# Optimization experiments

Measured on AMD Instinct MI355X. Metric: run time of the kernel, lower is better.

Reference implementation:

```python
import jax, jax.numpy as jnp
import numpy as np

B, L, D, V = 4096, 200, 64, 100000
ATTR_LEN = (2, 6, 10)  # label_size = 18
NEG = -1e9


def setup_inputs() -> dict:
    key = jax.random.key(0)
    ks = jax.random.split(key, 12)
    x = jax.random.randint(ks[0], (B, L), 0, V)
    lengths = jax.random.randint(ks[1], (B,), 1, L + 1)  # ragged valid lengths >= 1
    x_mask = jnp.arange(L)[None, :] < lengths[:, None]   # prefix-valid bool mask [B,L]
    y = (jax.random.uniform(ks[2], (B, sum(ATTR_LEN))) < 0.5).astype(jnp.float32)
    ob = (jax.random.uniform(ks[3], (B, sum(ATTR_LEN))) < 0.8).astype(jnp.float32)
    emb_table = (jax.random.normal(ks[4], (V, D)) * 0.02).at[0].set(0.0)  # padding_idx=0
    tran_W = jax.random.normal(ks[5], (3, D, D)) * 0.05   # emb_tran Linear weights (per attr)
    tran_b = jnp.zeros((3, D))
    att_W = jax.random.normal(ks[6], (3, D)) * 0.05       # item_att_W: Linear(D,1) per attr
    att_b = jnp.zeros((3,))
    W0 = jax.random.normal(ks[7], (D, ATTR_LEN[0])) * 0.05  # W_all (no bias)
    W1 = jax.random.normal(ks[8], (D, ATTR_LEN[1])) * 0.05
    W2 = jax.random.normal(ks[9], (D, ATTR_LEN[2])) * 0.05
    return {"x": x, "x_mask": x_mask, "y": y, "ob": ob, "emb_table": emb_table,
            "tran_W": tran_W, "tran_b": tran_b, "att_W": att_W, "att_b": att_b,
            "W0": W0, "W1": W1, "W2": W2}


def reference(x, x_mask, y, ob, emb_table, tran_W, tran_b, att_W, att_b, W0, W1, W2):
    # embed: [B,L,D]
    embed = emb_table[x]
    # per-attribute transformed embeddings: [3,B,L,D]
    e = jax.nn.relu(jnp.einsum('bld,ade->able', embed, tran_W) + tran_b[:, None, None, :])
    # attention logits per attribute: [3,B,L]
    att_u = jax.nn.relu(jnp.einsum('able,ae->abl', e, att_W) + att_b[:, None, None])
    # masked softmax over valid prefix (equivalent to the per-sample length loop)
    m = x_mask.astype(e.dtype)
    scores = jnp.where(x_mask[None, :, :], att_u, NEG)
    att = jax.nn.softmax(scores, axis=-1) * m[None, :, :]
    # attention-pooled user representation per attribute: [3,B,D]
    rep = jnp.tanh(jnp.einsum('abl,able->abe', att, e))
    # torch: cat([rep_a.unsqueeze(2)],2).view(B,-1) -> interleaved (d-major, attr-minor) layout
    user_flat = jnp.transpose(rep, (1, 2, 0)).reshape(rep.shape[1], -1)  # [B, 3*D]
    Ddim = emb_table.shape[1]
    W_user = jnp.concatenate([user_flat[:, 0 * Ddim:1 * Ddim] @ W0,
                              user_flat[:, 1 * Ddim:2 * Ddim] @ W1,
                              user_flat[:, 2 * Ddim:3 * Ddim] @ W2], axis=1)
    # W_compact = W_user * ob  (observed-label mask)
    return W_user * ob
```

## Files before the change

### kernel.cpp

```cpp
#include <hip/hip_runtime.h>

typedef unsigned int u32;
typedef unsigned short u16;
typedef unsigned char u8;
typedef unsigned long long u64;

typedef __attribute__((ext_vector_type(8))) short bf16x8;
typedef __attribute__((ext_vector_type(4))) float f32x4;
typedef __attribute__((ext_vector_type(4))) u32 u32x4;

#define L_SEQ 200
#define ST_ROWS 208
#define RND_MAX 9

__device__ __forceinline__ u16 f2bf(float f) {
    u32 u = __float_as_uint(f);
    return (u16)((u + 0x7FFFu + ((u >> 16) & 1u)) >> 16);
}
__device__ __forceinline__ u32 pk2bf(float fx, float fy) {
    u32 xb = __float_as_uint(fx) + 0x8000u;
    u32 yb = __float_as_uint(fy) + 0x8000u;
    return __byte_perm(xb, yb, 0x7632);
}

__device__ __forceinline__ float row16_sum(float v) {
    int x;
    x = __builtin_amdgcn_update_dpp(0, __float_as_int(v), 0x128, 0xF, 0xF, true);
    v += __int_as_float(x);
    x = __builtin_amdgcn_update_dpp(0, __float_as_int(v), 0x124, 0xF, 0xF, true);
    v += __int_as_float(x);
    x = __builtin_amdgcn_update_dpp(0, __float_as_int(v), 0x122, 0xF, 0xF, true);
    v += __int_as_float(x);
    x = __builtin_amdgcn_update_dpp(0, __float_as_int(v), 0x121, 0xF, 0xF, true);
    v += __int_as_float(x);
    return v;
}
__device__ __forceinline__ float wave_sumf(float v) {
    v = row16_sum(v);
    v += __shfl_xor(v, 16, 64);
    v += __shfl_xor(v, 32, 64);
    return v;
}

__global__ __launch_bounds__(256) void etna_prep(const void* __restrict__ xmask,
                                                 const float* __restrict__ tranW,
                                                 const float* __restrict__ emb,
                                                 void* __restrict__ ws, int Bn, int Vn,
                                                 int doConv) {
    const int tid = threadIdx.x;
    const int bid = blockIdx.x;

    if (doConv) {
        u64* dst = (u64*)((char*)ws + 40960);
        const float4* src = (const float4*)emb;
        int ng = Vn * 16;
        for (int i = bid * 256 + tid; i < ng; i += gridDim.x * 256) {
            float4 v = src[i];
            u64 lo = pk2bf(v.x, v.y);
            u64 hi = pk2bf(v.z, v.w);
            dst[i] = lo | (hi << 32);
        }
    }

    if (bid < 48) {
        int it = bid * 256 + tid;
        int jj = it & 7;
        int ln = (it >> 3) & 63;
        int kh = (it >> 9) & 1;
        int c = (it >> 10) & 3;
        int a = it >> 12;
        int k = kh * 32 + (ln >> 4) * 8 + jj;
        int n = c * 16 + (ln & 15);
        ((u16*)ws)[it] = f2bf(tranW[a * 4096 + k * 64 + n]);
        return;
    }

    const int wv = tid >> 6;
    const int lane = tid & 63;
    int esz;
    {
        u32 accF = 0, acc0 = 0, accO = 0;
#pragma unroll
        for (int k = 0; k < 4; ++k) {
            int i = lane + 64 * k;
            u32 w = (i < 200) ? ((const u32*)xmask)[i] : 0u;
            accF |= (w & 0xFEFEFEFEu);
            acc0 |= (w & 0x000000FFu);
            accO |= (w & 0xFFFFFF00u);
        }
        bool isFloat = __ballot(accF != 0) != 0;
        bool hasB0   = __ballot(acc0 != 0) != 0;
        bool hasOdd  = __ballot(accO != 0) != 0;
        esz = isFloat ? (hasB0 ? 2 : 4) : (hasOdd ? 1 : 4);
    }
    int s = (bid - 48) * 4 + wv;
    if (s < Bn) {
        int len = 0;
        int mbase = s * L_SEQ;
#pragma unroll
        for (int c4 = 0; c4 < 4; ++c4) {
            int l = c4 * 64 + lane;
            bool v = false;
            if (l < L_SEQ) {
                int off = mbase + l;
                if (esz == 1)      v = ((const u8*)xmask)[off] != 0;
                else if (esz == 2) v = ((const u16*)xmask)[off] != 0;
                else               v = ((const u32*)xmask)[off] != 0;
            }
            len += (int)__popcll(__ballot(v));
        }
        if (lane == 0) ((int*)((char*)ws + 24576))[s] = len;
    }
}

template <bool TAB>
__global__ __launch_bounds__(192, 4) void etna_mfma(
    const int* __restrict__ x, const float* __restrict__ ob,
    const float* __restrict__ emb, const float* __restrict__ tranb,
    const float* __restrict__ attW, const float* __restrict__ attb,
    const float* __restrict__ W0, const float* __restrict__ W1,
    const float* __restrict__ W2, float* __restrict__ out,
    const void* __restrict__ ws, int Vn) {
    __shared__ __align__(16) float ldsf[ST_ROWS * 32];
    char* ldsb = (char*)ldsf;

    const int tid = threadIdx.x;
    const int a = tid >> 6;
    const int lane = tid & 63;
    const int col = lane & 15;
    const int g = lane >> 4;
    const int b = blockIdx.x;

    const u16* wsBf = (const u16*)ws;
    bf16x8 Bf[4][2];
#pragma unroll
    for (int c = 0; c < 4; ++c)
#pragma unroll
        for (int kh = 0; kh < 2; ++kh)
            Bf[c][kh] = *(const bf16x8*)&wsBf[(((a * 4 + c) * 2 + kh) * 64 + lane) * 8];

    const int len = ((const int*)((const char*)ws + 24576))[b];
    const u16* wsEmb = (const u16*)((const char*)ws + 40960);

    const float LOG2E = 1.44269504088896f;
    float TB[4], AW[4];
#pragma unroll
    for (int c = 0; c < 4; ++c) {
        TB[c] = tranb[a * 64 + c * 16 + col];
        AW[c] = attW[a * 64 + c * 16 + col] * LOG2E;
    }
    const float AB = attb[a] * LOG2E;

    const int* xrow = x + b * L_SEQ;
    const int nt = (len + 15) >> 4;
    const int stRows = nt << 4;
    const int rounds = (stRows + 23) / 24;

    const int sp = a * 8 + (lane >> 3);
    const int ch = lane & 7;

    int ids[RND_MAX];
#pragma unroll
    for (int j = 0; j < RND_MAX; ++j) {
        ids[j] = 0;
        if (j < rounds) {
            int p = j * 24 + sp;
            int q = (p < L_SEQ) ? p : (L_SEQ - 1);
            int idv = xrow[q];
            idv = max(0, min(idv, Vn - 1));
            ids[j] = (p < len) ? idv : 0;
        }
    }

    if (TAB) {
        bf16x8 stq[3];
#pragma unroll
        for (int j = 0; j < RND_MAX + 2; ++j) {
            if (j < RND_MAX && j < rounds)
                stq[j % 3] = ((const bf16x8*)(wsEmb + (size_t)ids[j] * 64))[ch];
            int k = j - 2;
            if (k >= 0 && k < rounds) {
                int p = k * 24 + sp;
                if (p < stRows) {
                    u32 off = (u32)p * 128 + (u32)((ch * 16) ^ ((p & 7) << 4));
                    *(bf16x8*)(ldsb + off) = stq[k % 3];
                }
            }
        }
    } else {
        for (int j = 0; j < rounds; ++j) {
            int p = j * 24 + sp;
            if (p < stRows) {
                const float4* ep4 = (const float4*)(emb + (size_t)ids[j] * 64);
                float4 q0 = ep4[2 * ch], q1 = ep4[2 * ch + 1];
                u32x4 wv_;
                wv_.x = pk2bf(q0.x, q0.y);
                wv_.y = pk2bf(q0.z, q0.w);
                wv_.z = pk2bf(q1.x, q1.y);
                wv_.w = pk2bf(q1.z, q1.w);
                u32 off = (u32)p * 128 + (u32)((ch * 16) ^ ((p & 7) << 4));
                *(bf16x8*)(ldsb + off) = __builtin_bit_cast(bf16x8, wv_);
            }
        }
    }
    __syncthreads();

    const u32 c0 = (u32)((g * 16) ^ ((col & 7) << 4));
    u32 ra = (u32)col * 128 + c0;

    float NUM[4] = {0.f, 0.f, 0.f, 0.f};
    float DEN = 0.f;

    bf16x8 a0 = *(const bf16x8*)(ldsb + ra);
    bf16x8 a1 = *(const bf16x8*)(ldsb + (ra ^ 64u));

    for (int t = 0; t < nt; ++t) {
        bf16x8 n0 = a0, n1 = a1;
        if (t + 1 < nt) {
            u32 rn = ra + 2048u;
            n0 = *(const bf16x8*)(ldsb + rn);
            n1 = *(const bf16x8*)(ldsb + (rn ^ 64u));
        }
        ra += 2048u;

        f32x4 E[4];
#pragma unroll
        for (int c = 0; c < 4; ++c) {
            f32x4 cc = {TB[c], TB[c], TB[c], TB[c]};
            cc = __builtin_amdgcn_mfma_f32_16x16x32_bf16(a0, Bf[c][0], cc, 0, 0, 0);
            cc = __builtin_amdgcn_mfma_f32_16x16x32_bf16(a1, Bf[c][1], cc, 0, 0, 0);
            E[c].x = fmaxf(cc.x, 0.f);
            E[c].y = fmaxf(cc.y, 0.f);
            E[c].z = fmaxf(cc.z, 0.f);
            E[c].w = fmaxf(cc.w, 0.f);
        }
        float p0 = E[0].x * AW[0] + E[1].x * AW[1] + E[2].x * AW[2] + E[3].x * AW[3];
        float p1 = E[0].y * AW[0] + E[1].y * AW[1] + E[2].y * AW[2] + E[3].y * AW[3];
        float p2 = E[0].z * AW[0] + E[1].z * AW[1] + E[2].z * AW[2] + E[3].z * AW[3];
        float p3 = E[0].w * AW[0] + E[1].w * AW[1] + E[2].w * AW[2] + E[3].w * AW[3];
        p0 = row16_sum(p0);
        p1 = row16_sum(p1);
        p2 = row16_sum(p2);
        p3 = row16_sum(p3);

        int lrow = (t << 4) + 4 * g;
        float u0 = fmaxf(p0 + AB, 0.f);
        float u1 = fmaxf(p1 + AB, 0.f);
        float u2 = fmaxf(p2 + AB, 0.f);
        float u3 = fmaxf(p3 + AB, 0.f);
        float s0 = (lrow + 0 < len) ? exp2f(u0) : 0.f;
        float s1 = (lrow + 1 < len) ? exp2f(u1) : 0.f;
        float s2 = (lrow + 2 < len) ? exp2f(u2) : 0.f;
        float s3 = (lrow + 3 < len) ? exp2f(u3) : 0.f;
        DEN += s0 + s1 + s2 + s3;
#pragma unroll
        for (int c = 0; c < 4; ++c)
            NUM[c] += s0 * E[c].x + s1 * E[c].y + s2 * E[c].z + s3 * E[c].w;

        a0 = n0;
        a1 = n1;
    }

    __syncthreads();

    {
        float d = DEN;
        d += __shfl_xor(d, 16, 64);
        d += __shfl_xor(d, 32, 64);
        float rden = 1.0f / fmaxf(d, 1e-20f);
#pragma unroll
        for (int c = 0; c < 4; ++c) {
            float v = NUM[c];
            v += __shfl_xor(v, 16, 64);
            v += __shfl_xor(v, 32, 64);
            if (g == 0) ldsf[a * 64 + c * 16 + col] = tanhf(v * rden);
        }
    }
    __syncthreads();

    {
        const int AL = (a == 0) ? 2 : (a == 1 ? 6 : 10);
        const int OFF = (a == 0) ? 0 : (a == 1 ? 2 : 8);
        const float* Wp = (a == 0) ? W0 : (a == 1 ? W1 : W2);
        int gg = a * 64 + lane;
        float v = ldsf[(gg % 3) * 64 + gg / 3];
        for (int k = 0; k < AL; ++k) {
            float pz = wave_sumf(v * Wp[lane * AL + k]);
            if (lane == 0) out[b * 18 + OFF + k] = pz * ob[b * 18 + OFF + k];
        }
    }
}

extern "C" void kernel_launch(void* const* d_in, const int* in_sizes, int n_in,
                              void* d_out, int out_size, void* d_ws, size_t ws_size,
                              hipStream_t stream) {
    const int* x = (const int*)d_in[0];
    const void* xmask = d_in[1];
    const float* ob = (const float*)d_in[3];
    const float* emb = (const float*)d_in[4];
    const float* tranW = (const float*)d_in[5];
    const float* tranb = (const float*)d_in[6];
    const float* attW = (const float*)d_in[7];
    const float* attb = (const float*)d_in[8];
    const float* W0 = (const float*)d_in[9];
    const float* W1 = (const float*)d_in[10];
    const float* W2 = (const float*)d_in[11];

    const int Bn = in_sizes[0] / L_SEQ;
    const int Vn = in_sizes[4] / 64;

    const size_t need = 40960 + (size_t)Vn * 128;
    const int useTab = (ws_size >= need) ? 1 : 0;

    etna_prep<<<48 + (Bn + 3) / 4, 256, 0, stream>>>(xmask, tranW, emb, d_ws, Bn, Vn, useTab);
    if (useTab)
        etna_mfma<true><<<Bn, 192, 0, stream>>>(x, ob, emb, tranb, attW, attb,
                                                W0, W1, W2, (float*)d_out, d_ws, Vn);
    else
        etna_mfma<false><<<Bn, 192, 0, stream>>>(x, ob, emb, tranb, attW, attb,
                                                 W0, W1, W2, (float*)d_out, d_ws, Vn);
}
```

Measured before the change: 148.0 us.

## Split sequence tiles across two wave groups per attribute, doubling block size

Each block now launches 384 threads (six waves), and two waves share each attribute. Each wave handles half of the 16-row tiles, and the partial numerators and denominators are combined through shared memory. The gather uses twice as many threads per round, and the length mask is applied only in the final tile, so padded rows now load real ids. The output projection is spread over all six waves, one output per wave per round. The goal is to shorten the serial per-block MFMA loop and raise parallelism, at the cost of extra syncs and higher per-block register and LDS pressure.

```diff
diff --git a/kernel.cpp b/kernel.cpp
--- a/kernel.cpp
+++ b/kernel.cpp
@@ -11,7 +11,7 @@
 
 #define L_SEQ 200
 #define ST_ROWS 208
-#define RND_MAX 9
+#define RND_MAX 5
 
 __device__ __forceinline__ u16 f2bf(float f) {
     u32 u = __float_as_uint(f);
@@ -114,7 +114,7 @@
 }
 
 template <bool TAB>
-__global__ __launch_bounds__(192, 4) void etna_mfma(
+__global__ __launch_bounds__(384, 4) void etna_mfma(
     const int* __restrict__ x, const float* __restrict__ ob,
     const float* __restrict__ emb, const float* __restrict__ tranb,
     const float* __restrict__ attW, const float* __restrict__ attb,
@@ -122,10 +122,15 @@
     const float* __restrict__ W2, float* __restrict__ out,
     const void* __restrict__ ws, int Vn) {
     __shared__ __align__(16) float ldsf[ST_ROWS * 32];
+    __shared__ float pN[2][3][64];
+    __shared__ float pD[2][3];
+    __shared__ float rep[3][64];
     char* ldsb = (char*)ldsf;
 
     const int tid = threadIdx.x;
-    const int a = tid >> 6;
+    const int w = tid >> 6;
+    const int a = w % 3;
+    const int h = w / 3;
     const int lane = tid & 63;
     const int col = lane & 15;
     const int g = lane >> 4;
@@ -154,9 +159,9 @@
     const int* xrow = x + b * L_SEQ;
     const int nt = (len + 15) >> 4;
     const int stRows = nt << 4;
-    const int rounds = (stRows + 23) / 24;
-
-    const int sp = a * 8 + (lane >> 3);
+    const int rounds = (stRows + 47) / 48;
+
+    const int sp = w * 8 + (lane >> 3);
     const int ch = lane & 7;
 
     int ids[RND_MAX];
@@ -164,11 +169,10 @@
     for (int j = 0; j < RND_MAX; ++j) {
         ids[j] = 0;
         if (j < rounds) {
-            int p = j * 24 + sp;
+            int p = j * 48 + sp;
             int q = (p < L_SEQ) ? p : (L_SEQ - 1);
             int idv = xrow[q];
-            idv = max(0, min(idv, Vn - 1));
-            ids[j] = (p < len) ? idv : 0;
+            ids[j] = max(0, min(idv, Vn - 1));
         }
     }
 
@@ -180,7 +184,7 @@
                 stq[j % 3] = ((const bf16x8*)(wsEmb + (size_t)ids[j] * 64))[ch];
             int k = j - 2;
             if (k >= 0 && k < rounds) {
-                int p = k * 24 + sp;
+                int p = k * 48 + sp;
                 if (p < stRows) {
                     u32 off = (u32)p * 128 + (u32)((ch * 16) ^ ((p & 7) << 4));
                     *(bf16x8*)(ldsb + off) = stq[k % 3];
@@ -189,7 +193,7 @@
         }
     } else {
         for (int j = 0; j < rounds; ++j) {
-            int p = j * 24 + sp;
+            int p = j * 48 + sp;
             if (p < stRows) {
                 const float4* ep4 = (const float4*)(emb + (size_t)ids[j] * 64);
                 float4 q0 = ep4[2 * ch], q1 = ep4[2 * ch + 1];
@@ -205,18 +209,26 @@
     }
     __syncthreads();
 
+    const int nth = (nt + 1) >> 1;
+    const int tA = h * nth;
+    const int tB = min(nt, tA + nth);
+    const bool ownLast = (tB == nt) && (tA < tB);
+
     const u32 c0 = (u32)((g * 16) ^ ((col & 7) << 4));
-    u32 ra = (u32)col * 128 + c0;
+    u32 ra = (u32)(tA * 16 + col) * 128 + c0;
 
     float NUM[4] = {0.f, 0.f, 0.f, 0.f};
     float DEN = 0.f;
 
-    bf16x8 a0 = *(const bf16x8*)(ldsb + ra);
-    bf16x8 a1 = *(const bf16x8*)(ldsb + (ra ^ 64u));
-
-    for (int t = 0; t < nt; ++t) {
+    bf16x8 a0, a1;
+    if (tA < tB) {
+        a0 = *(const bf16x8*)(ldsb + ra);
+        a1 = *(const bf16x8*)(ldsb + (ra ^ 64u));
+    }
+
+    for (int t = tA; t < tB; ++t) {
         bf16x8 n0 = a0, n1 = a1;
-        if (t + 1 < nt) {
+        if (t + 1 < tB) {
             u32 rn = ra + 2048u;
             n0 = *(const bf16x8*)(ldsb + rn);
             n1 = *(const bf16x8*)(ldsb + (rn ^ 64u));
@@ -243,15 +255,17 @@
         p2 = row16_sum(p2);
         p3 = row16_sum(p3);
 
-        int lrow = (t << 4) + 4 * g;
-        float u0 = fmaxf(p0 + AB, 0.f);
-        float u1 = fmaxf(p1 + AB, 0.f);
-        float u2 = fmaxf(p2 + AB, 0.f);
-        float u3 = fmaxf(p3 + AB, 0.f);
-        float s0 = (lrow + 0 < len) ? exp2f(u0) : 0.f;
-        float s1 = (lrow + 1 < len) ? exp2f(u1) : 0.f;
-        float s2 = (lrow + 2 < len) ? exp2f(u2) : 0.f;
-        float s3 = (lrow + 3 < len) ? exp2f(u3) : 0.f;
+        float s0 = exp2f(fmaxf(p0 + AB, 0.f));
+        float s1 = exp2f(fmaxf(p1 + AB, 0.f));
+        float s2 = exp2f(fmaxf(p2 + AB, 0.f));
+        float s3 = exp2f(fmaxf(p3 + AB, 0.f));
+        if (ownLast && t == nt - 1) {
+            int lrow = (t << 4) + 4 * g;
+            s0 = (lrow + 0 < len) ? s0 : 0.f;
+            s1 = (lrow + 1 < len) ? s1 : 0.f;
+            s2 = (lrow + 2 < len) ? s2 : 0.f;
+            s3 = (lrow + 3 < len) ? s3 : 0.f;
+        }
         DEN += s0 + s1 + s2 + s3;
 #pragma unroll
         for (int c = 0; c < 4; ++c)
@@ -260,34 +274,41 @@
         a0 = n0;
         a1 = n1;
     }
-
-    __syncthreads();
 
     {
         float d = DEN;
         d += __shfl_xor(d, 16, 64);
         d += __shfl_xor(d, 32, 64);
-        float rden = 1.0f / fmaxf(d, 1e-20f);
+        if (lane == 0) pD[h][a] = d;
 #pragma unroll
         for (int c = 0; c < 4; ++c) {
             float v = NUM[c];
             v += __shfl_xor(v, 16, 64);
             v += __shfl_xor(v, 32, 64);
-            if (g == 0) ldsf[a * 64 + c * 16 + col] = tanhf(v * rden);
+            if (g == 0) pN[h][a][c * 16 + col] = v;
         }
     }
     __syncthreads();
 
-    {
-        const int AL = (a == 0) ? 2 : (a == 1 ? 6 : 10);
-        const int OFF = (a == 0) ? 0 : (a == 1 ? 2 : 8);
-        const float* Wp = (a == 0) ? W0 : (a == 1 ? W1 : W2);
-        int gg = a * 64 + lane;
-        float v = ldsf[(gg % 3) * 64 + gg / 3];
-        for (int k = 0; k < AL; ++k) {
-            float pz = wave_sumf(v * Wp[lane * AL + k]);
-            if (lane == 0) out[b * 18 + OFF + k] = pz * ob[b * 18 + OFF + k];
-        }
+    if (h == 0) {
+        float dt = pD[0][a] + pD[1][a];
+        float rden = 1.0f / fmaxf(dt, 1e-20f);
+        float nv = pN[0][a][lane] + pN[1][a][lane];
+        rep[a][lane] = tanhf(nv * rden);
+    }
+    __syncthreads();
+
+#pragma unroll
+    for (int r = 0; r < 3; ++r) {
+        int o = w + r * 6;
+        int seg = (o < 2) ? 0 : ((o < 8) ? 1 : 2);
+        int k = o - ((seg == 0) ? 0 : ((seg == 1) ? 2 : 8));
+        int AL = (seg == 0) ? 2 : ((seg == 1) ? 6 : 10);
+        const float* Wp = (seg == 0) ? W0 : ((seg == 1) ? W1 : W2);
+        int gg = seg * 64 + lane;
+        float v = rep[gg % 3][gg / 3];
+        float pz = wave_sumf(v * Wp[lane * AL + k]);
+        if (lane == 0) out[b * 18 + o] = pz * ob[b * 18 + o];
     }
 }
 
@@ -314,9 +335,9 @@
 
     etna_prep<<<48 + (Bn + 3) / 4, 256, 0, stream>>>(xmask, tranW, emb, d_ws, Bn, Vn, useTab);
     if (useTab)
-        etna_mfma<true><<<Bn, 192, 0, stream>>>(x, ob, emb, tranb, attW, attb,
+        etna_mfma<true><<<Bn, 384, 0, stream>>>(x, ob, emb, tranb, attW, attb,
                                                 W0, W1, W2, (float*)d_out, d_ws, Vn);
     else
-        etna_mfma<false><<<Bn, 192, 0, stream>>>(x, ob, emb, tranb, attW, attb,
+        etna_mfma<false><<<Bn, 384, 0, stream>>>(x, ob, emb, tranb, attW, attb,
                                                  W0, W1, W2, (float*)d_out, d_ws, Vn);
 }
```

Measured after the change: 166.1 us. +12.3%, slower.

## Stage embedding rows via direct global-to-LDS loads and rebalance epilogue

Applied to the files above, without the earlier changes.

Embedding rows are now copied straight from the bf16 table into LDS with global_load_lds, replacing the register-staged load-then-store pipeline. The XOR swizzle moves from the LDS destination address to the source chunk address. Separately, the sequence-length mask is applied only on the final tile, a separate rep buffer lets one barrier be dropped, and the 18 output dot-products are spread evenly across the three waves instead of waves doing 2, 6 or 10 each. The gain is lower VGPR use and fewer instructions, at the cost of relying on the implicit per-wave LDS layout of global_load_lds matching the swizzle.

```diff
diff --git a/kernel.cpp b/kernel.cpp
--- a/kernel.cpp
+++ b/kernel.cpp
@@ -21,6 +21,12 @@
     u32 xb = __float_as_uint(fx) + 0x8000u;
     u32 yb = __float_as_uint(fy) + 0x8000u;
     return __byte_perm(xb, yb, 0x7632);
+}
+
+__device__ __forceinline__ void gld_lds16(const void* g, void* l) {
+    __builtin_amdgcn_global_load_lds(
+        (const __attribute__((address_space(1))) u32*)g,
+        (__attribute__((address_space(3))) u32*)l, 16, 0, 0);
 }
 
 __device__ __forceinline__ float row16_sum(float v) {
@@ -122,6 +128,7 @@
     const float* __restrict__ W2, float* __restrict__ out,
     const void* __restrict__ ws, int Vn) {
     __shared__ __align__(16) float ldsf[ST_ROWS * 32];
+    __shared__ float rep[3][64];
     char* ldsb = (char*)ldsf;
 
     const int tid = threadIdx.x;
@@ -158,6 +165,7 @@
 
     const int sp = a * 8 + (lane >> 3);
     const int ch = lane & 7;
+    const u32 srcChunkOff = (u32)((ch ^ (lane >> 3)) << 4);
 
     int ids[RND_MAX];
 #pragma unroll
@@ -173,18 +181,15 @@
     }
 
     if (TAB) {
-        bf16x8 stq[3];
-#pragma unroll
-        for (int j = 0; j < RND_MAX + 2; ++j) {
-            if (j < RND_MAX && j < rounds)
-                stq[j % 3] = ((const bf16x8*)(wsEmb + (size_t)ids[j] * 64))[ch];
-            int k = j - 2;
-            if (k >= 0 && k < rounds) {
-                int p = k * 24 + sp;
-                if (p < stRows) {
-                    u32 off = (u32)p * 128 + (u32)((ch * 16) ^ ((p & 7) << 4));
-                    *(bf16x8*)(ldsb + off) = stq[k % 3];
-                }
+#pragma unroll
+        for (int j = 0; j < RND_MAX; ++j) {
+            if (j < rounds) {
+                int p = j * 24 + sp;
+                const char* gsrc =
+                    (const char*)wsEmb + (size_t)ids[j] * 128 + srcChunkOff;
+                char* ldst = ldsb + (u32)(j * 24 + a * 8) * 128;
+                if (p < stRows)
+                    gld_lds16(gsrc, ldst);
             }
         }
     } else {
@@ -243,15 +248,17 @@
         p2 = row16_sum(p2);
         p3 = row16_sum(p3);
 
-        int lrow = (t << 4) + 4 * g;
-        float u0 = fmaxf(p0 + AB, 0.f);
-        float u1 = fmaxf(p1 + AB, 0.f);
-        float u2 = fmaxf(p2 + AB, 0.f);
-        float u3 = fmaxf(p3 + AB, 0.f);
-        float s0 = (lrow + 0 < len) ? exp2f(u0) : 0.f;
-        float s1 = (lrow + 1 < len) ? exp2f(u1) : 0.f;
-        float s2 = (lrow + 2 < len) ? exp2f(u2) : 0.f;
-        float s3 = (lrow + 3 < len) ? exp2f(u3) : 0.f;
+        float s0 = exp2f(fmaxf(p0 + AB, 0.f));
+        float s1 = exp2f(fmaxf(p1 + AB, 0.f));
+        float s2 = exp2f(fmaxf(p2 + AB, 0.f));
+        float s3 = exp2f(fmaxf(p3 + AB, 0.f));
+        if (t == nt - 1) {
+            int lrow = (t << 4) + 4 * g;
+            s0 = (lrow + 0 < len) ? s0 : 0.f;
+            s1 = (lrow + 1 < len) ? s1 : 0.f;
+            s2 = (lrow + 2 < len) ? s2 : 0.f;
+            s3 = (lrow + 3 < len) ? s3 : 0.f;
+        }
         DEN += s0 + s1 + s2 + s3;
 #pragma unroll
         for (int c = 0; c < 4; ++c)
@@ -260,8 +267,6 @@
         a0 = n0;
         a1 = n1;
     }
-
-    __syncthreads();
 
     {
         float d = DEN;
@@ -273,21 +278,22 @@
             float v = NUM[c];
             v += __shfl_xor(v, 16, 64);
             v += __shfl_xor(v, 32, 64);
-            if (g == 0) ldsf[a * 64 + c * 16 + col] = tanhf(v * rden);
+            if (g == 0) rep[a][c * 16 + col] = tanhf(v * rden);
         }
     }
     __syncthreads();
 
-    {
-        const int AL = (a == 0) ? 2 : (a == 1 ? 6 : 10);
-        const int OFF = (a == 0) ? 0 : (a == 1 ? 2 : 8);
-        const float* Wp = (a == 0) ? W0 : (a == 1 ? W1 : W2);
-        int gg = a * 64 + lane;
-        float v = ldsf[(gg % 3) * 64 + gg / 3];
-        for (int k = 0; k < AL; ++k) {
-            float pz = wave_sumf(v * Wp[lane * AL + k]);
-            if (lane == 0) out[b * 18 + OFF + k] = pz * ob[b * 18 + OFF + k];
-        }
+#pragma unroll
+    for (int r = 0; r < 6; ++r) {
+        int o = a + 3 * r;
+        int seg = (o < 2) ? 0 : ((o < 8) ? 1 : 2);
+        int k = o - ((seg == 0) ? 0 : ((seg == 1) ? 2 : 8));
+        int AL = (seg == 0) ? 2 : ((seg == 1) ? 6 : 10);
+        const float* Wp = (seg == 0) ? W0 : ((seg == 1) ? W1 : W2);
+        int gg = seg * 64 + lane;
+        float v = rep[gg % 3][gg / 3];
+        float pz = wave_sumf(v * Wp[lane * AL + k]);
+        if (lane == 0) out[b * 18 + o] = pz * ob[b * 18 + o];
     }
 }
 
```

New measurement: 144.1 us. 2.7% less time.
